# Optimization experiments

Hardware: AMD Instinct MI355X
Metric: run time of the kernel (lower is better)

## Reference

```python
import jax, jax.numpy as jnp
import numpy as np

B, DIM, HEADS, Hs, Ws = 8, 192, 8, 128, 128


def setup_inputs() -> dict:
    key = jax.random.key(0)
    ks = jax.random.split(key, 8)
    d3 = 3 * DIM
    inp = {
        "x": jax.random.normal(ks[0], (B, DIM, Hs, Ws), dtype=jnp.float32),
        # qkv 1x1 conv: (out=3*dim, in=dim)
        "w_qkv": jax.random.normal(ks[1], (d3, DIM), dtype=jnp.float32) / np.sqrt(DIM),
        "b_qkv": jnp.zeros((d3,), dtype=jnp.float32),
        # depthwise 3x3 conv, groups = 3*dim -> kernel (3*dim, 1, 3, 3)
        "w_dw": jax.random.normal(ks[2], (d3, 1, 3, 3), dtype=jnp.float32) / 3.0,
        "b_dw": jnp.zeros((d3,), dtype=jnp.float32),
        # project_out 1x1 conv: (dim, dim)
        "w_proj": jax.random.normal(ks[3], (DIM, DIM), dtype=jnp.float32) / np.sqrt(DIM),
        "b_proj": jnp.zeros((DIM,), dtype=jnp.float32),
        "temperature": jnp.ones((HEADS, 1, 1), dtype=jnp.float32),
        "a1": jnp.full((1,), 0.2, dtype=jnp.float32),
        "a2": jnp.full((1,), 0.2, dtype=jnp.float32),
        "a3": jnp.full((1,), 0.2, dtype=jnp.float32),
        "a4": jnp.full((1,), 0.2, dtype=jnp.float32),
    }
    return inp


def _sparse_softmax(attn, k):
    # top-k per row, scatter 1s at those indices, mask rest to -inf, softmax
    _, idx = jax.lax.top_k(attn, k)                      # [..., C, k]
    C = attn.shape[-1]
    mask = jax.nn.one_hot(idx, C, dtype=attn.dtype).sum(-2)  # [..., C, C]
    masked = jnp.where(mask > 0, attn, -jnp.inf)
    return jax.nn.softmax(masked, axis=-1)


def _l2norm(t):
    # torch F.normalize: x / max(||x||_2, eps) along last axis
    n = jnp.sqrt(jnp.sum(t * t, axis=-1, keepdims=True))
    return t / jnp.maximum(n, 1e-12)


def reference(x, w_qkv, b_qkv, w_dw, b_dw, w_proj, b_proj, temperature, a1, a2, a3, a4):
    b, c, h, w = x.shape
    # 1x1 conv
    qkv = jnp.einsum('oi,bihw->bohw', w_qkv, x) + b_qkv[:, None, None]
    # depthwise 3x3 conv, padding=1
    qkv = jax.lax.conv_general_dilated(
        qkv, w_dw, window_strides=(1, 1), padding='SAME',
        feature_group_count=3 * c,
        dimension_numbers=('NCHW', 'OIHW', 'NCHW')) + b_dw[:, None, None]
    q, k, v = jnp.split(qkv, 3, axis=1)
    Cd = c // HEADS  # per-head channel dim
    heads = lambda t: t.reshape(b, HEADS, Cd, h * w)
    q, k, v = heads(q), heads(k), heads(v)
    q, k = _l2norm(q), _l2norm(k)
    # transposed (channel) attention: [b, head, Cd, Cd]
    attn = jnp.einsum('bhcn,bhdn->bhcd', q, k) * temperature
    ks = (int(Cd / 2), int(Cd * 2 / 3), int(Cd * 3 / 4), int(Cd * 4 / 5))
    out1 = jnp.einsum('bhcd,bhdn->bhcn', _sparse_softmax(attn, ks[0]), v)
    out2 = jnp.einsum('bhcd,bhdn->bhcn', _sparse_softmax(attn, ks[1]), v)
    out3 = jnp.einsum('bhcd,bhdn->bhcn', _sparse_softmax(attn, ks[2]), v)
    out4 = jnp.einsum('bhcd,bhdn->bhcn', _sparse_softmax(attn, ks[3]), v)
    out = out1 * a1 + out2 * a2 + out3 * a3 + out4 * a4
    out = out.reshape(b, c, h, w)
    out = jnp.einsum('oi,bihw->bohw', w_proj, out) + b_proj[:, None, None]
    return out
```

## Files before the change

### kernel.cpp

```cpp
#include <hip/hip_runtime.h>
#include <math.h>

#define DIMC 192
#define C3 576
#define NHEADS 8
#define CDh 24
#define HWN 16384
#define WIDTH 128
#define NBATCH 8

typedef __attribute__((ext_vector_type(8))) short short8;
typedef __attribute__((ext_vector_type(4))) float f32x4;

__device__ __forceinline__ ushort f2bf(float f) {
    uint u = __float_as_uint(f);
    u += 0x7fff + ((u >> 16) & 1);
    return (ushort)(u >> 16);
}
__device__ __forceinline__ float bf2f(ushort h) {
    return __uint_as_float(((uint)h) << 16);
}

__global__ void k0_prep(const float* __restrict__ W, ushort* __restrict__ Wh,
                        ushort* __restrict__ Wl, int n) {
    int i = blockIdx.x * 256 + threadIdx.x;
    if (i < n) {
        float w = W[i];
        ushort h = f2bf(w);
        Wh[i] = h;
        Wl[i] = f2bf(w - bf2f(h));
    }
}

__global__ __launch_bounds__(256, 2) void kgx9(const float* __restrict__ x,
                                               const ushort* __restrict__ Wh,
                                               const ushort* __restrict__ Wl,
                                               const float* __restrict__ bias,
                                               float* __restrict__ qkv, long qkv_zs) {
    __shared__ ushort smem[2 * 64 * 200];
    ushort* BsH = smem;
    ushort* BsL = smem + 64 * 200;
    const int z = blockIdx.z;
    const float* xb = x + (size_t)z * DIMC * HWN;
    const int n0 = blockIdx.x * 64;
    const int tid = threadIdx.x;
#pragma unroll
    for (int it = 0; it < 12; it++) {
        int idx = tid + it * 256;
        int ch = idx >> 4, q = idx & 15;
        f32x4 v = *(const f32x4*)&xb[(size_t)ch * HWN + n0 + q * 4];
#pragma unroll
        for (int p = 0; p < 4; p++) {
            ushort hb = f2bf(v[p]);
            BsH[(q * 4 + p) * 200 + ch] = hb;
            BsL[(q * 4 + p) * 200 + ch] = f2bf(v[p] - bf2f(hb));
        }
    }
    __syncthreads();
    const int wid = tid >> 6, lane = tid & 63;
    const int lr = lane & 15, lk = lane >> 4;
    const int mb = wid * 144;
    float* oz = qkv + (size_t)z * qkv_zs;
    f32x4 acc[9][4];
#pragma unroll
    for (int i = 0; i < 9; i++)
#pragma unroll
        for (int j = 0; j < 4; j++) acc[i][j] = (f32x4)0.f;

    for (int kc6 = 0; kc6 < 6; kc6++) {
        short8 bh[4], bl[4];
#pragma unroll
        for (int j = 0; j < 4; j++) {
            int ad = (j * 16 + lr) * 200 + kc6 * 32 + lk * 8;
            bh[j] = *(const short8*)&BsH[ad];
            bl[j] = *(const short8*)&BsL[ad];
        }
#pragma unroll
        for (int i = 0; i < 9; i++) {
            size_t ao = (size_t)(mb + i * 16 + lr) * DIMC + kc6 * 32 + lk * 8;
            const short8 ah = *(const short8*)&Wh[ao];
            const short8 al = *(const short8*)&Wl[ao];
#pragma unroll
            for (int j = 0; j < 4; j++) {
                acc[i][j] = __builtin_amdgcn_mfma_f32_16x16x32_bf16(ah, bh[j], acc[i][j], 0, 0, 0);
                acc[i][j] = __builtin_amdgcn_mfma_f32_16x16x32_bf16(ah, bl[j], acc[i][j], 0, 0, 0);
                acc[i][j] = __builtin_amdgcn_mfma_f32_16x16x32_bf16(al, bh[j], acc[i][j], 0, 0, 0);
            }
        }
    }
    __syncthreads();
    float* epsb = (float*)smem + wid * (2 * 1056);
#pragma unroll
    for (int i = 0; i < 9; i++) {
        float* eps = epsb + (i & 1) * 1056;
        int rb = mb + i * 16;
#pragma unroll
        for (int j = 0; j < 4; j++)
#pragma unroll
            for (int r = 0; r < 4; r++)
                eps[(lk * 4 + r) * 66 + j * 16 + lr] = acc[i][j][r] + bias[rb + lk * 4 + r];
#pragma unroll
        for (int s = 0; s < 4; s++) {
            int rl = s * 4 + (lane >> 4);
            int c4 = (lane & 15) * 4;
            f32x4 v = *(const f32x4*)&eps[rl * 66 + c4];
            *(f32x4*)&oz[(size_t)(rb + rl) * HWN + n0 + c4] = v;
        }
    }
}

__global__ __launch_bounds__(256, 3) void kg3f(float* __restrict__ vy,
                                               const ushort* __restrict__ Mh,
                                               const ushort* __restrict__ Ml,
                                               const float* __restrict__ bias) {
    __shared__ ushort smem[2 * 64 * 200];
    ushort* BsH = smem;
    ushort* BsL = smem + 64 * 200;
    const int z = blockIdx.y;
    float* vb = vy + (size_t)z * DIMC * HWN;
    const int n0 = blockIdx.x * 64;
    const int tid = threadIdx.x;
#pragma unroll
    for (int it = 0; it < 12; it++) {
        int idx = tid + it * 256;
        int ch = idx >> 4, q = idx & 15;
        f32x4 v = *(const f32x4*)&vb[(size_t)ch * HWN + n0 + q * 4];
#pragma unroll
        for (int p = 0; p < 4; p++) {
            ushort hb = f2bf(v[p]);
            BsH[(q * 4 + p) * 200 + ch] = hb;
            BsL[(q * 4 + p) * 200 + ch] = f2bf(v[p] - bf2f(hb));
        }
    }
    __syncthreads();
    const int wid = tid >> 6, lane = tid & 63;
    const int lr = lane & 15, lk = lane >> 4;
    const int mb = wid * 48;
    const ushort* Azh = Mh + (size_t)z * DIMC * DIMC;
    const ushort* Azl = Ml + (size_t)z * DIMC * DIMC;
    f32x4 acc[3][4];
#pragma unroll
    for (int i = 0; i < 3; i++)
#pragma unroll
        for (int j = 0; j < 4; j++) acc[i][j] = (f32x4)0.f;

    for (int kc6 = 0; kc6 < 6; kc6++) {
        short8 bh[4], bl[4];
#pragma unroll
        for (int j = 0; j < 4; j++) {
            int ad = (j * 16 + lr) * 200 + kc6 * 32 + lk * 8;
            bh[j] = *(const short8*)&BsH[ad];
            bl[j] = *(const short8*)&BsL[ad];
        }
#pragma unroll
        for (int i = 0; i < 3; i++) {
            size_t ao = (size_t)(mb + i * 16 + lr) * DIMC + kc6 * 32 + lk * 8;
            const short8 ah = *(const short8*)&Azh[ao];
            const short8 al = *(const short8*)&Azl[ao];
#pragma unroll
            for (int j = 0; j < 4; j++) {
                acc[i][j] = __builtin_amdgcn_mfma_f32_16x16x32_bf16(ah, bh[j], acc[i][j], 0, 0, 0);
                acc[i][j] = __builtin_amdgcn_mfma_f32_16x16x32_bf16(ah, bl[j], acc[i][j], 0, 0, 0);
                acc[i][j] = __builtin_amdgcn_mfma_f32_16x16x32_bf16(al, bh[j], acc[i][j], 0, 0, 0);
            }
        }
    }
    __syncthreads();
    float* epsb = (float*)smem + wid * (2 * 1056);
#pragma unroll
    for (int i = 0; i < 3; i++) {
        float* eps = epsb + (i & 1) * 1056;
        int rb = mb + i * 16;
#pragma unroll
        for (int j = 0; j < 4; j++)
#pragma unroll
            for (int r = 0; r < 4; r++)
                eps[(lk * 4 + r) * 66 + j * 16 + lr] = acc[i][j][r] + bias[rb + lk * 4 + r];
#pragma unroll
        for (int s = 0; s < 4; s++) {
            int rl = s * 4 + (lane >> 4);
            int c4 = (lane & 15) * 4;
            f32x4 v = *(const f32x4*)&eps[rl * 66 + c4];
            *(f32x4*)&vb[(size_t)(rb + rl) * HWN + n0 + c4] = v;
        }
    }
}

__global__ __launch_bounds__(1024, 4) void k2_dw(const float* __restrict__ qkv0, long qkv_zs,
                                                 const float* __restrict__ wdw,
                                                 const float* __restrict__ bdw,
                                                 float* __restrict__ vout,
                                                 float* __restrict__ part, int b0) {
    __shared__ float stage[2 * 6336];
    __shared__ float qks[48 * 520];
    const int b = b0 + blockIdx.z;
    const float* qkv = qkv0 + (size_t)blockIdx.z * qkv_zs;
    const int stripe = blockIdx.x, h = blockIdx.y;
    const int tid = threadIdx.x;
    const int r0 = stripe * 4;

    const int col4 = (tid & 31) * 4;
    const int orow = (tid >> 5) & 3;
    const int cc = tid >> 7;

    auto stage_load = [&](int chunk, int buf) {
        const int g = chunk / 3, cb = (chunk % 3) * 8;
        float* sb = stage + buf * 6336;
#pragma unroll
        for (int f = tid; f < 1536; f += 1024) {
            int fc = f / 192, rem = f - fc * 192;
            int rl = rem >> 5, c4 = rem & 31;
            int gr = r0 - 1 + rl;
            int ch = g * DIMC + h * CDh + cb + fc;
            float4 v = make_float4(0.f, 0.f, 0.f, 0.f);
            if (gr >= 0 && gr < 128)
                v = *(const float4*)&qkv[(size_t)ch * HWN + gr * WIDTH + c4 * 4];
            *(float4*)&sb[(fc * 6 + rl) * 132 + c4 * 4] = v;
        }
    };

    stage_load(0, 0);
    __syncthreads();
    for (int chunk = 0; chunk < 9; chunk++) {
        const int buf = chunk & 1;
        if (chunk < 8) stage_load(chunk + 1, buf ^ 1);
        const int g = chunk / 3, cb = (chunk % 3) * 8;
        const float* sb = stage + buf * 6336;
        const int ch = g * DIMC + h * CDh + cb + cc;
        float wr[9];
#pragma unroll
        for (int t = 0; t < 9; t++) wr[t] = wdw[ch * 9 + t];
        float bsv = bdw[ch];
        float a0 = bsv, a1 = bsv, a2 = bsv, a3 = bsv;
#pragma unroll
        for (int dr = 0; dr < 3; dr++) {
            const float* row = &sb[(cc * 6 + orow + dr) * 132];
            f32x4 cen = *(const f32x4*)&row[col4];
            f32x4 lf4 = (col4 > 0) ? *(const f32x4*)&row[col4 - 4] : (f32x4)0.f;
            f32x4 rt4 = (col4 < 124) ? *(const f32x4*)&row[col4 + 4] : (f32x4)0.f;
            float left = lf4[3], right = rt4[0];
            float wA = wr[dr * 3 + 0], wB = wr[dr * 3 + 1], wC = wr[dr * 3 + 2];
            a0 = fmaf(left, wA, fmaf(cen[0], wB, fmaf(cen[1], wC, a0)));
            a1 = fmaf(cen[0], wA, fmaf(cen[1], wB, fmaf(cen[2], wC, a1)));
            a2 = fmaf(cen[1], wA, fmaf(cen[2], wB, fmaf(cen[3], wC, a2)));
            a3 = fmaf(cen[2], wA, fmaf(cen[3], wB, fmaf(right, wC, a3)));
        }
        if (g < 2) {
            float4 o4 = {a0, a1, a2, a3};
            *(float4*)&qks[(g * CDh + cb + cc) * 520 + orow * 128 + col4] = o4;
        } else {
            float4 o4 = {a0, a1, a2, a3};
            *(float4*)&vout[((size_t)b * DIMC + h * CDh + cb + cc) * HWN +
                            (size_t)(r0 + orow) * WIDTH + col4] = o4;
        }
        __syncthreads();
    }

    const int tc = tid & 3, td = (tid >> 2) & 3, tp = tid >> 4;
    float ga[6][6];
#pragma unroll
    for (int i = 0; i < 6; i++)
#pragma unroll
        for (int j = 0; j < 6; j++) ga[i][j] = 0.f;
#pragma unroll
    for (int s = 0; s < 2; s++) {
        int px = tp * 8 + s * 4;
        f32x4 qv[6], kv[6];
#pragma unroll
        for (int i = 0; i < 6; i++) qv[i] = *(const f32x4*)&qks[(tc * 6 + i) * 520 + px];
#pragma unroll
        for (int j = 0; j < 6; j++) kv[j] = *(const f32x4*)&qks[(24 + td * 6 + j) * 520 + px];
#pragma unroll
        for (int i = 0; i < 6; i++)
#pragma unroll
            for (int j = 0; j < 6; j++) {
                ga[i][j] = fmaf(qv[i][0], kv[j][0], ga[i][j]);
                ga[i][j] = fmaf(qv[i][1], kv[j][1], ga[i][j]);
                ga[i][j] = fmaf(qv[i][2], kv[j][2], ga[i][j]);
                ga[i][j] = fmaf(qv[i][3], kv[j][3], ga[i][j]);
            }
    }
#pragma unroll
    for (int i = 0; i < 6; i++)
#pragma unroll
        for (int j = 0; j < 6; j++) {
            float v = ga[i][j];
            v += __shfl_xor(v, 16, 64);
            v += __shfl_xor(v, 32, 64);
            ga[i][j] = v;
        }
    float nv = 0.f;
    int nch = 0, npg = 0;
    if (tid < 768) {
        npg = tid / 48;
        nch = tid - npg * 48;
#pragma unroll
        for (int s = 0; s < 8; s++) {
            f32x4 v = *(const f32x4*)&qks[nch * 520 + npg * 32 + s * 4];
            nv = fmaf(v[0], v[0], nv);
            nv = fmaf(v[1], v[1], nv);
            nv = fmaf(v[2], v[2], nv);
            nv = fmaf(v[3], v[3], nv);
        }
    }
    __syncthreads();
    float* gscr = qks;
    const int wave = tid >> 6;
    if ((tid & 63) < 16) {
#pragma unroll
        for (int i = 0; i < 6; i++)
#pragma unroll
            for (int j = 0; j < 6; j++)
                gscr[wave * 624 + (tc * 6 + i) * 24 + (td * 6 + j)] = ga[i][j];
    }
    if (tid < 768) gscr[npg * 624 + 576 + nch] = nv;
    __syncthreads();
    if (tid < 624) {
        float s = 0.f;
#pragma unroll
        for (int w2 = 0; w2 < 16; w2++) s += gscr[w2 * 624 + tid];
        part[((size_t)(b * NHEADS + h) * 64 + stripe) * 624 + tid] = s;
    }
}

__global__ void k34_attn(const float* __restrict__ part, const float* __restrict__ temp,
                         const float* __restrict__ a1, const float* __restrict__ a2,
                         const float* __restrict__ a3, const float* __restrict__ a4,
                         float* __restrict__ Aeff) {
    __shared__ float gbuf[624];
    int bh = blockIdx.x;
    int h = bh & 7;
    int tid = threadIdx.x;
    for (int ti = tid; ti < 624; ti += 256) {
        float s = 0.f;
        const float* p = part + (size_t)bh * 64 * 624 + ti;
#pragma unroll 4
        for (int st = 0; st < 64; st++) s += p[st * 624];
        gbuf[ti] = s;
    }
    __syncthreads();
    int r = tid;
    if (r >= CDh) return;
    float t = temp[h];
    float aw[4] = {a1[0], a2[0], a3[0], a4[0]};
    const int kks[4] = {12, 16, 18, 19};
    float qn = fmaxf(sqrtf(gbuf[576 + r]), 1e-12f);
    float av[24];
    for (int d = 0; d < 24; d++) {
        float kn = fmaxf(sqrtf(gbuf[600 + d]), 1e-12f);
        av[d] = gbuf[r * 24 + d] / (qn * kn) * t;
    }
    int rank[24];
    float m = -1e30f;
    for (int d = 0; d < 24; d++) {
        int rk = 0;
        for (int e = 0; e < 24; e++)
            rk += (av[e] > av[d]) || (av[e] == av[d] && e < d);
        rank[d] = rk;
        m = fmaxf(m, av[d]);
    }
    float ex[24], outv[24];
    for (int d = 0; d < 24; d++) { ex[d] = expf(av[d] - m); outv[d] = 0.f; }
    for (int i = 0; i < 4; i++) {
        float Z = 0.f;
        for (int d = 0; d < 24; d++) if (rank[d] < kks[i]) Z += ex[d];
        float inv = aw[i] / Z;
        for (int d = 0; d < 24; d++) if (rank[d] < kks[i]) outv[d] += ex[d] * inv;
    }
    for (int d = 0; d < 24; d++) Aeff[(bh * 24 + r) * 24 + d] = outv[d];
}

__global__ void k4b_mmat(const float* __restrict__ Wp, const float* __restrict__ Aeff,
                         ushort* __restrict__ Mh, ushort* __restrict__ Ml) {
    int b = blockIdx.x;
    int e0 = blockIdx.y * 6144;
    for (int e = e0 + threadIdx.x; e < e0 + 6144; e += 256) {
        int o = e / DIMC, j = e % DIMC;
        int h = j / CDh, d = j % CDh;
        const float* wrow = Wp + o * DIMC + h * CDh;
        const float* acol = Aeff + (size_t)((b * NHEADS + h) * CDh) * CDh + d;
        float s = 0.f;
        for (int c = 0; c < CDh; c++) s = fmaf(wrow[c], acol[c * CDh], s);
        size_t idx = ((size_t)b * DIMC + o) * DIMC + j;
        ushort hb = f2bf(s);
        Mh[idx] = hb;
        Ml[idx] = f2bf(s - bf2f(hb));
    }
}

extern "C" void kernel_launch(void* const* d_in, const int* in_sizes, int n_in,
                              void* d_out, int out_size, void* d_ws, size_t ws_size,
                              hipStream_t stream) {
    const float* x     = (const float*)d_in[0];
    const float* wqkv  = (const float*)d_in[1];
    const float* bqkv  = (const float*)d_in[2];
    const float* wdw   = (const float*)d_in[3];
    const float* bdw   = (const float*)d_in[4];
    const float* wproj = (const float*)d_in[5];
    const float* bproj = (const float*)d_in[6];
    const float* temp  = (const float*)d_in[7];
    const float* a1    = (const float*)d_in[8];
    const float* a2    = (const float*)d_in[9];
    const float* a3    = (const float*)d_in[10];
    const float* a4    = (const float*)d_in[11];
    float* out = (float*)d_out;

    float* ws = (float*)d_ws;
    const size_t fl_part = (size_t)64 * 64 * 624;
    const size_t fl_A    = (size_t)64 * 576;
    const size_t fl_M    = (size_t)NBATCH * DIMC * DIMC / 2;
    const size_t fl_W    = (size_t)C3 * DIMC / 2;
    const size_t fl_qkv1 = (size_t)C3 * HWN;
    const size_t base_fl = fl_part + fl_A + 2 * fl_M + 2 * fl_W;

    auto need = [&](int nzz) -> size_t {
        return (base_fl + (size_t)nzz * fl_qkv1) * sizeof(float);
    };
    int nz = 1;
    if (ws_size >= need(8))      nz = 8;
    else if (ws_size >= need(4)) nz = 4;
    else if (ws_size >= need(2)) nz = 2;

    size_t o = 0;
    float* part = ws + o; o += fl_part;
    float* Aeff = ws + o; o += fl_A;
    ushort* Mh  = (ushort*)(ws + o); o += fl_M;
    ushort* Ml  = (ushort*)(ws + o); o += fl_M;
    ushort* Wh  = (ushort*)(ws + o); o += fl_W;
    ushort* Wl  = (ushort*)(ws + o); o += fl_W;
    float* qkv  = ws + o;

    const long qkv_zs = (long)fl_qkv1;

    k0_prep<<<(C3 * DIMC + 255) / 256, 256, 0, stream>>>(wqkv, Wh, Wl, C3 * DIMC);

    for (int b0 = 0; b0 < NBATCH; b0 += nz) {
        kgx9<<<dim3(256, 1, nz), 256, 0, stream>>>(x + (size_t)b0 * DIMC * HWN,
                                                   Wh, Wl, bqkv, qkv, qkv_zs);
        k2_dw<<<dim3(32, 8, nz), 1024, 0, stream>>>(qkv, qkv_zs, wdw, bdw, out, part, b0);
    }
    k34_attn<<<64, 256, 0, stream>>>(part, temp, a1, a2, a3, a4, Aeff);
    k4b_mmat<<<dim3(8, 6), 256, 0, stream>>>(wproj, Aeff, Mh, Ml);
    kg3f<<<dim3(256, 8), 256, 0, stream>>>(out, Mh, Ml, bproj);
}
```

Measured before the change: 512.9 us.

## Process one batch per launch and split QKV GEMM output channels across blocks

The QKV 1x1-conv GEMM kernel now has each block compute 192 output channels, 48 per wave, over a grid of 256x3. Before, each block computed all 576 channels, and a variable number of batches ran per launch depending on workspace size. The host loop now always launches one batch at a time, so the qkv buffer is sized for a single batch and stays small enough that it may remain L2/LLC resident between the GEMM and depthwise kernels. The split lowers register pressure (acc[3][4] instead of acc[9][4]) and allows 3 blocks per CU. The cost is that each block re-stages and re-converts x three times, and every batch needs two smaller launches, which gives less parallelism per launch.

```diff
diff --git a/kernel.cpp b/kernel.cpp
--- a/kernel.cpp
+++ b/kernel.cpp
@@ -32,23 +32,22 @@
     }
 }
 
-__global__ __launch_bounds__(256, 2) void kgx9(const float* __restrict__ x,
+__global__ __launch_bounds__(256, 3) void kgx3(const float* __restrict__ x,
                                                const ushort* __restrict__ Wh,
                                                const ushort* __restrict__ Wl,
                                                const float* __restrict__ bias,
-                                               float* __restrict__ qkv, long qkv_zs) {
+                                               float* __restrict__ qkv) {
     __shared__ ushort smem[2 * 64 * 200];
     ushort* BsH = smem;
     ushort* BsL = smem + 64 * 200;
-    const int z = blockIdx.z;
-    const float* xb = x + (size_t)z * DIMC * HWN;
     const int n0 = blockIdx.x * 64;
+    const int o0 = blockIdx.y * 192;
     const int tid = threadIdx.x;
 #pragma unroll
     for (int it = 0; it < 12; it++) {
         int idx = tid + it * 256;
         int ch = idx >> 4, q = idx & 15;
-        f32x4 v = *(const f32x4*)&xb[(size_t)ch * HWN + n0 + q * 4];
+        f32x4 v = *(const f32x4*)&x[(size_t)ch * HWN + n0 + q * 4];
 #pragma unroll
         for (int p = 0; p < 4; p++) {
             ushort hb = f2bf(v[p]);
@@ -59,11 +58,10 @@
     __syncthreads();
     const int wid = tid >> 6, lane = tid & 63;
     const int lr = lane & 15, lk = lane >> 4;
-    const int mb = wid * 144;
-    float* oz = qkv + (size_t)z * qkv_zs;
-    f32x4 acc[9][4];
-#pragma unroll
-    for (int i = 0; i < 9; i++)
+    const int mb = o0 + wid * 48;
+    f32x4 acc[3][4];
+#pragma unroll
+    for (int i = 0; i < 3; i++)
 #pragma unroll
         for (int j = 0; j < 4; j++) acc[i][j] = (f32x4)0.f;
 
@@ -76,7 +74,7 @@
             bl[j] = *(const short8*)&BsL[ad];
         }
 #pragma unroll
-        for (int i = 0; i < 9; i++) {
+        for (int i = 0; i < 3; i++) {
             size_t ao = (size_t)(mb + i * 16 + lr) * DIMC + kc6 * 32 + lk * 8;
             const short8 ah = *(const short8*)&Wh[ao];
             const short8 al = *(const short8*)&Wl[ao];
@@ -91,7 +89,7 @@
     __syncthreads();
     float* epsb = (float*)smem + wid * (2 * 1056);
 #pragma unroll
-    for (int i = 0; i < 9; i++) {
+    for (int i = 0; i < 3; i++) {
         float* eps = epsb + (i & 1) * 1056;
         int rb = mb + i * 16;
 #pragma unroll
@@ -104,7 +102,7 @@
             int rl = s * 4 + (lane >> 4);
             int c4 = (lane & 15) * 4;
             f32x4 v = *(const f32x4*)&eps[rl * 66 + c4];
-            *(f32x4*)&oz[(size_t)(rb + rl) * HWN + n0 + c4] = v;
+            *(f32x4*)&qkv[(size_t)(rb + rl) * HWN + n0 + c4] = v;
         }
     }
 }
@@ -186,15 +184,13 @@
     }
 }
 
-__global__ __launch_bounds__(1024, 4) void k2_dw(const float* __restrict__ qkv0, long qkv_zs,
+__global__ __launch_bounds__(1024, 4) void k2_dw(const float* __restrict__ qkv,
                                                  const float* __restrict__ wdw,
                                                  const float* __restrict__ bdw,
                                                  float* __restrict__ vout,
-                                                 float* __restrict__ part, int b0) {
+                                                 float* __restrict__ part, int b) {
     __shared__ float stage[2 * 6336];
     __shared__ float qks[48 * 520];
-    const int b = b0 + blockIdx.z;
-    const float* qkv = qkv0 + (size_t)blockIdx.z * qkv_zs;
     const int stripe = blockIdx.x, h = blockIdx.y;
     const int tid = threadIdx.x;
     const int r0 = stripe * 4;
@@ -411,15 +407,6 @@
     const size_t fl_M    = (size_t)NBATCH * DIMC * DIMC / 2;
     const size_t fl_W    = (size_t)C3 * DIMC / 2;
     const size_t fl_qkv1 = (size_t)C3 * HWN;
-    const size_t base_fl = fl_part + fl_A + 2 * fl_M + 2 * fl_W;
-
-    auto need = [&](int nzz) -> size_t {
-        return (base_fl + (size_t)nzz * fl_qkv1) * sizeof(float);
-    };
-    int nz = 1;
-    if (ws_size >= need(8))      nz = 8;
-    else if (ws_size >= need(4)) nz = 4;
-    else if (ws_size >= need(2)) nz = 2;
 
     size_t o = 0;
     float* part = ws + o; o += fl_part;
@@ -429,15 +416,14 @@
     ushort* Wh  = (ushort*)(ws + o); o += fl_W;
     ushort* Wl  = (ushort*)(ws + o); o += fl_W;
     float* qkv  = ws + o;
-
-    const long qkv_zs = (long)fl_qkv1;
+    (void)fl_qkv1;
 
     k0_prep<<<(C3 * DIMC + 255) / 256, 256, 0, stream>>>(wqkv, Wh, Wl, C3 * DIMC);
 
-    for (int b0 = 0; b0 < NBATCH; b0 += nz) {
-        kgx9<<<dim3(256, 1, nz), 256, 0, stream>>>(x + (size_t)b0 * DIMC * HWN,
-                                                   Wh, Wl, bqkv, qkv, qkv_zs);
-        k2_dw<<<dim3(32, 8, nz), 1024, 0, stream>>>(qkv, qkv_zs, wdw, bdw, out, part, b0);
+    for (int b = 0; b < NBATCH; b++) {
+        kgx3<<<dim3(256, 3), 256, 0, stream>>>(x + (size_t)b * DIMC * HWN,
+                                               Wh, Wl, bqkv, qkv);
+        k2_dw<<<dim3(32, 8), 1024, 0, stream>>>(qkv, wdw, bdw, out, part, b);
     }
     k34_attn<<<64, 256, 0, stream>>>(part, temp, a1, a2, a3, a4, Aeff);
     k4b_mmat<<<dim3(8, 6), 256, 0, stream>>>(wproj, Aeff, Mh, Ml);
```

Result: faster. 493.7 us (-3.7%).
